# Optimization experiments

Hardware: AMD Instinct MI355X
Metric: run time of the kernel (lower is better)

## Reference

```python
import jax, jax.numpy as jnp
import numpy as np

TIME_NUM, WEEK_NUM = 288, 7
HID = 32          # hid_dim
T_OUT, IN_DIM = 12, 3
RF_DIM = 64       # random_feature_dim
TAU = 1.0
EPS_RF = 1e-6
EPS_LN = 1e-5


def _make_proj(m, d, seed=0):
    """Performer random matrix: stacked rows of QR-orthogonalized dxd blocks,
    scaled by chi-distributed row norms (create_random_matrix, scaling=0)."""
    rng = np.random.RandomState(seed)
    blocks = []
    for _ in range(m // d):
        q, _ = np.linalg.qr(rng.randn(d, d))
        blocks.append(q.T)
    rem = m - (m // d) * d
    if rem > 0:
        q, _ = np.linalg.qr(rng.randn(d, d))
        blocks.append(q.T[:rem])
    mat = np.vstack(blocks)
    mult = np.linalg.norm(rng.randn(m, d), axis=1)
    return jnp.asarray((mult[:, None] * mat).astype(np.float32))


def setup_inputs() -> dict:
    key = jax.random.key(0)
    B, N = 4, 50000
    ks = iter(jax.random.split(key, 40))
    rn = lambda *s: jax.random.normal(next(ks), s, jnp.float32) * 0.1
    inp = {
        "x": jax.random.uniform(next(ks), (B, N, T_OUT, IN_DIM), jnp.float32),
        "node_emb": rn(N, HID),
        "time_emb": rn(TIME_NUM, HID),
        "week_emb": rn(WEEK_NUM, HID),
        "W_in": rn(HID, T_OUT * IN_DIM), "b_in": rn(HID),
        "W1": rn(HID, 3 * HID), "b1": rn(HID),
        "W2": rn(HID, 3 * HID), "b2": rn(HID),
        "W_reg": rn(T_OUT, 8 * HID), "b_reg": rn(T_OUT),
        "proj": _make_proj(RF_DIM, HID, 0),
    }
    for i in range(2):
        inp[f"fc_in{i}_w"] = rn(4 * HID, 4 * HID)
        inp[f"fc_in{i}_b"] = rn(4 * HID)
        inp[f"fc_out{i}_w"] = rn(4 * HID, 4 * HID)
        inp[f"fc_out{i}_b"] = rn(4 * HID)
        inp[f"ln{i}_g"] = jnp.ones(4 * HID, jnp.float32)
        inp[f"ln{i}_b"] = jnp.zeros(4 * HID, jnp.float32)
    return inp


def _rf_map(data, proj, is_query):
    # data: [B,N,H,D], proj: [M,D] -> features [B,N,H,M]
    d = data.shape[-1]
    data = data * (float(d) ** -0.25)
    ratio = 1.0 / jnp.sqrt(jnp.asarray(proj.shape[0], data.dtype))
    dash = jnp.einsum('bnhd,md->bnhm', data, proj)
    diag = jnp.sum(data * data, -1, keepdims=True) * 0.5
    mx = jnp.max(dash, -1, keepdims=True)
    if not is_query:
        mx = jnp.max(mx, 1, keepdims=True)  # also max over nodes (dim -3)
    return ratio * (jnp.exp(dash - diag - mx) + EPS_RF)


def _linear_kernel(x, q, k):
    # x: [B,N,H,D], q/k: [B,N,H,M] -> O(N) kernelized attention
    v2x = jnp.einsum('bnhm,bnhd->bhmd', k, x)
    out1 = jnp.einsum('bnhm,bhmd->bnhd', q, v2x)
    ksum = jnp.sum(k, axis=1)                       # [B,H,M]
    out2 = jnp.einsum('bnhm,bhm->bnh', q, ksum)[..., None]
    return out1 / out2


def _layernorm(h, g, b):
    mu = jnp.mean(h, -1, keepdims=True)
    var = jnp.mean((h - mu) ** 2, -1, keepdims=True)
    return (h - mu) * jax.lax.rsqrt(var + EPS_LN) * g + b


def _forward(x, node_emb, time_emb, week_emb, W_in, b_in, W1, b1, W2, b2,
             W_reg, b_reg, proj,
             fc_in0_w, fc_in0_b, fc_out0_w, fc_out0_b, ln0_g, ln0_b,
             fc_in1_w, fc_in1_b, fc_out1_w, fc_out1_b, ln1_g, ln1_b):
    B, N, T, D = x.shape
    time_idx = jnp.clip((x[:, :, -1, 1] * TIME_NUM).astype(jnp.int32), 0, TIME_NUM - 1)
    week_idx = jnp.clip(x[:, :, -1, 2].astype(jnp.int32), 0, WEEK_NUM - 1)
    te = time_emb[time_idx]                                  # [B,N,H]
    we = week_emb[week_idx]                                  # [B,N,H]
    ne = jnp.broadcast_to(node_emb[None], (B, N, HID))       # [B,N,H]
    inp = x.reshape(B, N, T * D) @ W_in.T + b_in             # 1x1 conv == matmul
    xg = jnp.concatenate([ne, te, we], -1)                   # [B,N,3H]
    h = jnp.concatenate([inp, ne, te, we], -1)               # [B,N,4H]

    inv_sqrt_tau = 1.0 / float(np.sqrt(TAU))
    nv1 = ((xg @ W1.T + b1) * inv_sqrt_tau)[:, :, None, :]   # [B,N,1,H]
    nv2 = ((xg @ W2.T + b2) * inv_sqrt_tau)[:, :, None, :]
    q = _rf_map(nv1, proj, True)                             # [B,N,1,M]
    k = _rf_map(nv2, proj, False)

    layers = [(fc_in0_w, fc_in0_b, fc_out0_w, fc_out0_b, ln0_g, ln0_b),
              (fc_in1_w, fc_in1_b, fc_out1_w, fc_out1_b, ln1_g, ln1_b)]
    h0 = h
    for wi, bi, wo, bo, g, bt in layers:
        res = h
        v = jax.nn.sigmoid(h @ wi.T + bi) * (h @ wo.T + bo)  # GLU; dropout=eval
        v = _linear_kernel(v[:, :, None, :], q, k)[:, :, 0, :]
        h = _layernorm(v + res, g, bt)

    out = jax.nn.relu(jnp.concatenate([h0, h], -1))          # [B,N,8H]
    out = out @ W_reg.T + b_reg                              # [B,N,T_out]
    return jnp.swapaxes(out, 1, 2)                           # [B,T_out,N]


def reference(x, node_emb, time_emb, week_emb, W_in, b_in, W1, b1, W2, b2,
              W_reg, b_reg, proj,
              fc_in0_w, fc_in0_b, fc_out0_w, fc_out0_b, ln0_g, ln0_b,
              fc_in1_w, fc_in1_b, fc_out1_w, fc_out1_b, ln1_g, ln1_b):
    return _forward(x, node_emb, time_emb, week_emb, W_in, b_in, W1, b1, W2, b2,
                    W_reg, b_reg, proj,
                    fc_in0_w, fc_in0_b, fc_out0_w, fc_out0_b, ln0_g, ln0_b,
                    fc_in1_w, fc_in1_b, fc_out1_w, fc_out1_b, ln1_g, ln1_b)
```

## Files before the change

kernel.cpp:

```cpp
#include <hip/hip_runtime.h>

#define NB 4
#define NN 50000
#define NT 784

#define H0B    0L
#define H1B    51200000L
#define QB     102400000L
#define KKB    128000000L
#define RMB    153600000L
#define WBFB   154400000L
#define V2F0B  154531072L
#define V2F1B  154662144L
#define KSB    154793216L
#define GMB    154794240L
#define W12B   154795264L
#define V2TB   154819840L
#define NZERO  65796

typedef short short8_t __attribute__((ext_vector_type(8)));
typedef float f32x4 __attribute__((ext_vector_type(4)));

__device__ __forceinline__ unsigned short f2bf(float f){
  unsigned u = __float_as_uint(f);
  return (unsigned short)((u + 0x7FFFu + ((u>>16)&1u)) >> 16);
}
__device__ __forceinline__ float bf2f(unsigned short s){
  return __uint_as_float(((unsigned)s)<<16);
}
__device__ __forceinline__ unsigned pk2(float a, float b){
  return (unsigned)f2bf(a) | ((unsigned)f2bf(b)<<16);
}
__device__ __forceinline__ uint4 pk8(const float* f){
  uint4 o; o.x=pk2(f[0],f[1]); o.y=pk2(f[2],f[3]);
  o.z=pk2(f[4],f[5]); o.w=pk2(f[6],f[7]); return o;
}
__device__ __forceinline__ void up8(uint4 v, float* f){
  f[0]=bf2f((unsigned short)(v.x&0xFFFFu)); f[1]=bf2f((unsigned short)(v.x>>16));
  f[2]=bf2f((unsigned short)(v.y&0xFFFFu)); f[3]=bf2f((unsigned short)(v.y>>16));
  f[4]=bf2f((unsigned short)(v.z&0xFFFFu)); f[5]=bf2f((unsigned short)(v.z>>16));
  f[6]=bf2f((unsigned short)(v.w&0xFFFFu)); f[7]=bf2f((unsigned short)(v.w>>16));
}
__device__ __forceinline__ short8_t relu8(short8_t s){
  short8_t r;
  #pragma unroll
  for (int i=0;i<8;i++){ short v = s[i]; r[i] = (v & (short)0x8000) ? (short)0 : v; }
  return r;
}
__device__ __forceinline__ unsigned encOrd(float f){
  unsigned u = __float_as_uint(f);
  return (u & 0x80000000u) ? ~u : (u | 0x80000000u);
}
__device__ __forceinline__ float decOrd(unsigned u){
  return (u & 0x80000000u) ? __uint_as_float(u & 0x7fffffffu)
                           : __uint_as_float(~u);
}

__global__ void k_init(char* __restrict__ wsb){
  int i = blockIdx.x*256 + threadIdx.x;
  if (i < NZERO) ((unsigned*)(wsb + V2F0B))[i] = 0u;
}
__global__ void k_wcvt(const float* __restrict__ wi0, const float* __restrict__ wo0,
                       const float* __restrict__ wi1, const float* __restrict__ wo1,
                       char* __restrict__ wsb){
  int idx = blockIdx.x*256 + threadIdx.x;
  if (idx >= 65536) return;
  int l = idx >> 15, r = (idx >> 7) & 255, c = idx & 127;
  const float* src = (l==0) ? ((r<128)? wi0 : wo0) : ((r<128)? wi1 : wo1);
  float v = src[(r&127)*128 + c];
  ((unsigned short*)(wsb + WBFB))[l*32768 + r*128 + c] = f2bf(v);
}
__global__ void k_wcvt2(const float* __restrict__ W1, const float* __restrict__ W2,
                        const float* __restrict__ proj, const float* __restrict__ W_reg,
                        char* __restrict__ wsb){
  int i = blockIdx.x*256 + threadIdx.x;
  if (i >= 12288) return;
  unsigned short* dst = (unsigned short*)(wsb + W12B);
  float v;
  if (i < 3072) v = W1[i];
  else if (i < 6144) v = W2[i-3072];
  else if (i < 8192) v = proj[i-6144];
  else {
    int r = (i-8192) >> 8, c = (i-8192) & 255;
    v = (r < 12) ? W_reg[r*256 + c] : 0.f;
  }
  dst[i] = f2bf(v);
}

__global__ __launch_bounds__(256) void k_pass1a(
  const float* __restrict__ x, const float* __restrict__ node_emb,
  const float* __restrict__ time_emb, const float* __restrict__ week_emb,
  const float* __restrict__ W_in, const float* __restrict__ b_in,
  char* __restrict__ wsb)
{
  const int b = blockIdx.y;
  const int n = blockIdx.x*256 + threadIdx.x;
  if (n >= NN) return;
  const long row = (long)b*NN + n;
  float xr[36];
  {
    const float4* xp = (const float4*)(x + row*36);
    #pragma unroll
    for (int i=0;i<9;i++){ float4 t=xp[i]; xr[4*i]=t.x; xr[4*i+1]=t.y; xr[4*i+2]=t.z; xr[4*i+3]=t.w; }
  }
  int tidx = (int)(xr[34]*288.0f); tidx = tidx<0?0:(tidx>287?287:tidx);
  int widx = (int)(xr[35]);        widx = widx<0?0:(widx>6?6:widx);
  uint4* h0q = (uint4*)(wsb + H0B) + row*16;
  float hh[32];
  #pragma unroll 1
  for (int jj=0;jj<8;jj++){
    #pragma unroll
    for (int jl=0;jl<4;jl++){
      const int j = jj*4+jl;
      const float* w = W_in + j*36;
      float a0=0.f,a1=0.f,a2=0.f,a3=0.f;
      #pragma unroll
      for (int i=0;i<36;i+=4){ a0+=xr[i]*w[i]; a1+=xr[i+1]*w[i+1]; a2+=xr[i+2]*w[i+2]; a3+=xr[i+3]*w[i+3]; }
      hh[j] = b_in[j] + ((a0+a1)+(a2+a3));
    }
  }
  #pragma unroll
  for (int c=0;c<4;c++) h0q[c] = pk8(hh + 8*c);
  float xg[96];
  {
    const float4* p0 = (const float4*)(node_emb + (long)n*32);
    const float4* p1 = (const float4*)(time_emb + (long)tidx*32);
    const float4* p2 = (const float4*)(week_emb + (long)widx*32);
    #pragma unroll
    for (int i=0;i<8;i++){ float4 t=p0[i]; xg[4*i]=t.x; xg[4*i+1]=t.y; xg[4*i+2]=t.z; xg[4*i+3]=t.w; }
    #pragma unroll
    for (int i=0;i<8;i++){ float4 t=p1[i]; xg[32+4*i]=t.x; xg[32+4*i+1]=t.y; xg[32+4*i+2]=t.z; xg[32+4*i+3]=t.w; }
    #pragma unroll
    for (int i=0;i<8;i++){ float4 t=p2[i]; xg[64+4*i]=t.x; xg[64+4*i+1]=t.y; xg[64+4*i+2]=t.z; xg[64+4*i+3]=t.w; }
  }
  #pragma unroll
  for (int c=0;c<12;c++) h0q[4+c] = pk8(xg + 8*c);
}

__global__ __launch_bounds__(256) void k_pass1b(
  const float* __restrict__ b1, const float* __restrict__ b2,
  char* __restrict__ wsb)
{
  __shared__ unsigned short xgt[64][104];
  __shared__ unsigned short dt[2][64][40];
  __shared__ unsigned short ot[64][72];
  __shared__ unsigned short w1l[32][104];
  __shared__ unsigned short w2l[32][104];
  __shared__ unsigned short pjl[64][40];
  __shared__ float wred[4];
  const int b   = blockIdx.y;
  const int tid = threadIdx.x;
  const int lane= tid & 63;
  const int w   = tid >> 6;
  const int c   = lane & 15;
  const int kg  = lane >> 4;
  const int nblk = gridDim.x;
  const int srow = tid >> 2, sq3 = tid & 3;
  {
    const unsigned short* w1bf = (const unsigned short*)(wsb + W12B);
    const unsigned short* w2bf = w1bf + 3072;
    const unsigned short* pjbf = w1bf + 6144;
    for (int i = tid; i < 3072; i += 256){ w1l[i/96][i%96] = w1bf[i]; w2l[i/96][i%96] = w2bf[i]; }
    for (int i = tid; i < 2048; i += 256){ pjl[i/32][i%32] = pjbf[i]; }
  }
  uint4 xv0, xv1, xv2;
  {
    const long r0 = (long)blockIdx.x*64;
    long gr = r0 + srow;
    xv0=(uint4){0,0,0,0}; xv1=xv0; xv2=xv0;
    if (gr < NN){
      const uint4* src = (const uint4*)(wsb + H0B + ((long)b*NN + gr)*256 + 64 + sq3*48);
      xv0=src[0]; xv1=src[1]; xv2=src[2];
    }
  }
  #pragma unroll 1
  for (int tile = blockIdx.x; tile < NT; tile += nblk){
    const long r0blk = (long)tile*64;
    {
      uint4* d = (uint4*)&xgt[srow][sq3*24];
      d[0]=xv0; d[1]=xv1; d[2]=xv2;
    }
    if (tile + nblk < NT){
      const long r1 = (long)(tile + nblk)*64;
      long gr = r1 + srow;
      xv0=(uint4){0,0,0,0}; xv1=xv0; xv2=xv0;
      if (gr < NN){
        const uint4* src = (const uint4*)(wsb + H0B + ((long)b*NN + gr)*256 + 64 + sq3*48);
        xv0=src[0]; xv1=src[1]; xv2=src[2];
      }
    }
    __syncthreads();
    f32x4 accd[2][2];
    #pragma unroll
    for (int s=0;s<2;s++)
      #pragma unroll
      for (int f=0;f<2;f++) accd[s][f] = (f32x4){0.f,0.f,0.f,0.f};
    #pragma unroll
    for (int ks=0;ks<3;ks++){
      short8_t a = *(const short8_t*)&xgt[w*16 + c][ks*32 + kg*8];
      #pragma unroll
      for (int f=0;f<2;f++){
        short8_t bw1 = *(const short8_t*)&w1l[f*16+c][ks*32 + kg*8];
        accd[0][f] = __builtin_amdgcn_mfma_f32_16x16x32_bf16(a, bw1, accd[0][f], 0,0,0);
        short8_t bw2 = *(const short8_t*)&w2l[f*16+c][ks*32 + kg*8];
        accd[1][f] = __builtin_amdgcn_mfma_f32_16x16x32_bf16(a, bw2, accd[1][f], 0,0,0);
      }
    }
    const float DSC = 0.42044820762685725f;
    float dv[2][2][4];
    #pragma unroll
    for (int f=0;f<2;f++){
      float bb1 = b1[f*16+c], bb2 = b2[f*16+c];
      #pragma unroll
      for (int jj=0;jj<4;jj++){
        dv[0][f][jj] = (accd[0][f][jj] + bb1) * DSC;
        dv[1][f][jj] = (accd[1][f][jj] + bb2) * DSC;
      }
    }
    float dg[2][4];
    #pragma unroll
    for (int s=0;s<2;s++)
      #pragma unroll
      for (int jj=0;jj<4;jj++){
        float t = dv[s][0][jj]*dv[s][0][jj] + dv[s][1][jj]*dv[s][1][jj];
        #pragma unroll
        for (int off=1; off<16; off<<=1) t += __shfl_xor(t, off);
        dg[s][jj] = 0.5f * t;
      }
    #pragma unroll
    for (int s=0;s<2;s++)
      #pragma unroll
      for (int f=0;f<2;f++)
        #pragma unroll
        for (int jj=0;jj<4;jj++)
          dt[s][w*16 + kg*4 + jj][f*16 + c] = f2bf(dv[s][f][jj]);
    __syncthreads();
    f32x4 acc2[2][4];
    #pragma unroll
    for (int s=0;s<2;s++){
      short8_t ad = *(const short8_t*)&dt[s][w*16 + c][kg*8];
      #pragma unroll
      for (int f=0;f<4;f++){
        short8_t bp = *(const short8_t*)&pjl[f*16+c][kg*8];
        acc2[s][f] = __builtin_amdgcn_mfma_f32_16x16x32_bf16(ad, bp, (f32x4){0.f,0.f,0.f,0.f}, 0,0,0);
      }
    }
    float mx[2][4];
    #pragma unroll
    for (int s=0;s<2;s++)
      #pragma unroll
      for (int jj=0;jj<4;jj++){
        float t = fmaxf(fmaxf(acc2[s][0][jj],acc2[s][1][jj]),
                        fmaxf(acc2[s][2][jj],acc2[s][3][jj]));
        #pragma unroll
        for (int off=1; off<16; off<<=1) t = fmaxf(t, __shfl_xor(t, off));
        mx[s][jj] = t;
      }
    #pragma unroll
    for (int f=0;f<4;f++)
      #pragma unroll
      for (int jj=0;jj<4;jj++){
        float qv = 0.125f*(__expf(acc2[0][f][jj] - dg[0][jj] - mx[0][jj]) + 1e-6f);
        ot[w*16 + kg*4 + jj][f*16 + c] = f2bf(qv);
      }
    __syncthreads();
    {
      long gr = r0blk + srow;
      if (gr < NN){
        const uint4* s = (const uint4*)&ot[srow][sq3*16];
        uint4* dst = (uint4*)((unsigned short*)(wsb + QB) + ((long)b*NN + gr)*64 + sq3*16);
        dst[0] = s[0]; dst[1] = s[1];
      }
    }
    __syncthreads();
    float bmax = -3.0e38f;
    #pragma unroll
    for (int f=0;f<4;f++)
      #pragma unroll
      for (int jj=0;jj<4;jj++){
        float kv = __expf(acc2[1][f][jj] - mx[1][jj]);
        ot[w*16 + kg*4 + jj][f*16 + c] = f2bf(kv);
      }
    #pragma unroll
    for (int jj=0;jj<4;jj++){
      long gr = r0blk + w*16 + kg*4 + jj;
      bool val = (gr < NN);
      if (val && c==0)
        ((float*)(wsb + RMB))[(long)b*NN + gr] = mx[1][jj] - dg[1][jj];
      if (val) bmax = fmaxf(bmax, mx[1][jj]);
    }
    #pragma unroll
    for (int off=32; off>0; off>>=1) bmax = fmaxf(bmax, __shfl_xor(bmax, off));
    if (lane==0) wred[w] = bmax;
    __syncthreads();
    {
      long gr = r0blk + srow;
      if (gr < NN){
        const uint4* s = (const uint4*)&ot[srow][sq3*16];
        uint4* dst = (uint4*)((unsigned short*)(wsb + KKB) + ((long)b*NN + gr)*64 + sq3*16);
        dst[0] = s[0]; dst[1] = s[1];
      }
    }
    if (tid==0){
      float m2 = fmaxf(fmaxf(wred[0],wred[1]), fmaxf(wred[2],wred[3]));
      atomicMax((unsigned*)(wsb + GMB) + b, encOrd(m2));
    }
    __syncthreads();
  }
}

__global__ __launch_bounds__(256) void k_glured(
  char* __restrict__ wsb, const unsigned short* __restrict__ hsrc,
  const unsigned short* __restrict__ wbf,
  const float* __restrict__ bi, const float* __restrict__ bo,
  float* __restrict__ v2x_out, float* __restrict__ ksout)
{
  __shared__ unsigned short ht[64][132];
  __shared__ unsigned short htT[128][72];
  __shared__ unsigned short ktl[2][64][72];
  __shared__ float red[256];
  extern __shared__ unsigned short wl[];
  const int b = blockIdx.y;
  const int tid = threadIdx.x;
  const int lane = tid & 63;
  const int w = tid >> 6;
  const int c = lane & 15;
  const int kg = lane >> 4;
  const int nblk = gridDim.x;
  const float gm = decOrd(((const unsigned*)(wsb + GMB))[b]);
  const float* rm = (const float*)(wsb + RMB) + (long)b*NN;
  const uint4* kbase = (const uint4*)(wsb + KKB) + (long)b*NN*8;
  {
    uint4* wl4 = (uint4*)wl;
    const uint4* src = (const uint4*)wbf;
    #pragma unroll
    for (int e=0;e<16;e++){
      int i = tid + 256*e;
      int row = i >> 4, blk = i & 15;
      wl4[row*16 + (blk ^ (row & 7))] = src[i];
    }
  }
  f32x4 racc[8];
  #pragma unroll
  for (int f=0;f<8;f++) racc[f] = (f32x4){0.f,0.f,0.f,0.f};
  float ksacc = 0.f;
  float bi_l[8], bo_l[8];
  #pragma unroll
  for (int f=0;f<8;f++){ bi_l[f] = bi[f*16+c]; bo_l[f] = bo[f*16+c]; }
  const int krr = tid>>3, kcc = tid&7;
  const int srow = tid>>2, sq3 = tid&3;
  const int rswz = ((w*16 + c) >> 3) & 7;
  const int wswz = c & 7;
  uint4 hv0,hv1,hv2,hv3, krA,krB; float rmA,rmB;
  {
    const long r0 = (long)blockIdx.x*64;
    long gr = r0 + srow;
    hv0=(uint4){0,0,0,0}; hv1=hv0; hv2=hv0; hv3=hv0;
    if (gr < NN){
      const uint4* s = (const uint4*)(hsrc + ((long)b*NN + gr)*128 + sq3*32);
      hv0=s[0]; hv1=s[1]; hv2=s[2]; hv3=s[3];
    }
    krA=(uint4){0,0,0,0}; krB=krA; rmA=0.f; rmB=0.f;
    long gA = r0 + krr;      if (gA < NN){ krA = kbase[gA*8 + kcc]; rmA = rm[gA]; }
    long gB = r0 + krr + 32; if (gB < NN){ krB = kbase[gB*8 + kcc]; rmB = rm[gB]; }
  }
  int p = 0;
  #pragma unroll 1
  for (int tile = blockIdx.x; tile < NT; tile += nblk){
    const long r0 = (long)tile*64;
    {
      uint4* d = (uint4*)&ht[srow][sq3*32];
      d[0]=hv0; d[1]=hv1; d[2]=hv2; d[3]=hv3;
    }
    {
      bool vA = (r0 + krr) < NN;
      bool vB = (r0 + krr + 32) < NN;
      float sA = __expf(rmA - gm), sB = __expf(rmB - gm);
      float ta[8], tb[8];
      up8(krA, ta); up8(krB, tb);
      #pragma unroll
      for (int i=0;i<8;i++){
        ta[i] = vA ? 0.125f*(ta[i]*sA + 1e-6f) : 0.f;
        tb[i] = vB ? 0.125f*(tb[i]*sB + 1e-6f) : 0.f;
      }
      const int pA = (((krr>>3) ^ kcc) << 3) | (krr & 7);
      const int pB = ((((krr>>3)+4) ^ kcc) << 3) | (krr & 7);
      #pragma unroll
      for (int i=0;i<8;i++){
        ktl[p][kcc*8+i][pA] = f2bf(ta[i]);
        ktl[p][kcc*8+i][pB] = f2bf(tb[i]);
      }
    }
    if (tile + nblk < NT){
      const long r1 = (long)(tile + nblk)*64;
      long gr = r1 + srow;
      hv0=(uint4){0,0,0,0}; hv1=hv0; hv2=hv0; hv3=hv0;
      if (gr < NN){
        const uint4* s = (const uint4*)(hsrc + ((long)b*NN + gr)*128 + sq3*32);
        hv0=s[0]; hv1=s[1]; hv2=s[2]; hv3=s[3];
      }
      krA=(uint4){0,0,0,0}; krB=krA; rmA=0.f; rmB=0.f;
      long gA = r1 + krr;      if (gA < NN){ krA = kbase[gA*8 + kcc]; rmA = rm[gA]; }
      long gB = r1 + krr + 32; if (gB < NN){ krB = kbase[gB*8 + kcc]; rmB = rm[gB]; }
    }
    __syncthreads();
    f32x4 gacc[16];
    #pragma unroll
    for (int f=0;f<16;f++) gacc[f] = (f32x4){0.f,0.f,0.f,0.f};
    #pragma unroll
    for (int ks=0;ks<4;ks++){
      short8_t a = *(const short8_t*)&ht[w*16 + c][ks*32 + kg*8];
      #pragma unroll
      for (int f=0;f<16;f++){
        short8_t bb = *(const short8_t*)(wl + (((f*16 + c)*16 + ((ks*4 + kg) ^ wswz)) << 3));
        gacc[f] = __builtin_amdgcn_mfma_f32_16x16x32_bf16(a, bb, gacc[f], 0, 0, 0);
      }
    }
    #pragma unroll
    for (int f=0;f<8;f++)
      #pragma unroll
      for (int j=0;j<4;j++){
        float aa = gacc[f][j]   + bi_l[f];
        float cc2= gacc[f+8][j] + bo_l[f];
        float o  = cc2 / (1.0f + __expf(-aa));
        bool val = (r0 + w*16 + kg*4 + j) < NN;
        htT[f*16 + c][w*16 + kg*4 + j] = val ? f2bf(o) : (unsigned short)0;
      }
    if (ksout){
      int m = tid & 63, n0 = (tid>>6)*16;
      int sm = (m>>3)&7;
      #pragma unroll
      for (int n=0;n<16;n++){
        int nn = n0+n;
        ksacc += bf2f(ktl[p][m][(((nn>>3)^sm)<<3)|(nn&7)]);
      }
    }
    __syncthreads();
    #pragma unroll
    for (int ks=0;ks<2;ks++){
      short8_t a = *(const short8_t*)&ktl[p][w*16 + c][((ks*4 + kg) ^ rswz) << 3];
      #pragma unroll
      for (int f=0;f<8;f++){
        short8_t bb = *(const short8_t*)&htT[f*16 + c][ks*32 + kg*8];
        racc[f] = __builtin_amdgcn_mfma_f32_16x16x32_bf16(a, bb, racc[f], 0, 0, 0);
      }
    }
    p ^= 1;
  }
  float* v2x = v2x_out + (long)b*8192;
  #pragma unroll
  for (int f=0;f<8;f++)
    #pragma unroll
    for (int j=0;j<4;j++)
      atomicAdd(&v2x[(w*16 + kg*4 + j)*128 + f*16 + c], racc[f][j]);
  if (ksout){
    red[tid] = ksacc;
    __syncthreads();
    if (tid < 64)
      atomicAdd(ksout + b*64 + tid,
                red[tid]+red[64+tid]+red[128+tid]+red[192+tid]);
  }
}

__global__ void k_v2cvt(char* __restrict__ wsb, const float* __restrict__ v2f){
  int idx = blockIdx.x*256 + threadIdx.x;
  if (idx >= 36864) return;
  int b = idx / 9216, rem = idx % 9216;
  int n = rem / 64, m = rem % 64;
  const float* ks = (const float*)(wsb + KSB);
  float v = (n < 128) ? v2f[b*8192 + m*128 + n] : ((n==128) ? ks[b*64+m] : 0.f);
  ((unsigned short*)(wsb + V2TB))[b*9216 + n*64 + m] = f2bf(v);
}

__global__ __launch_bounds__(256) void k_attnln(
  char* __restrict__ wsb, const float* __restrict__ g0,
  const float* __restrict__ bt0)
{
  __shared__ unsigned short ht[64][132];
  __shared__ unsigned short v2s[144*72];
  const int b = blockIdx.y;
  const int tid = threadIdx.x;
  const int lane = tid & 63;
  const int w  = tid >> 6;
  const int c  = lane & 15;
  const int kg = lane >> 4;
  const int nblk = gridDim.x;
  const int rrow = tid>>2, rq3 = tid&3;
  const unsigned short* qb = (const unsigned short*)(wsb + QB) + (long)b*NN*64;
  const unsigned short* h0g = (const unsigned short*)(wsb + H0B) + (long)b*NN*128;
  unsigned short* h1g = (unsigned short*)(wsb + H1B) + (long)b*NN*128;
  {
    const uint4* v2g = (const uint4*)((const unsigned short*)(wsb + V2TB) + b*9216);
    #pragma unroll
    for (int e=0;e<5;e++){
      int j = tid + 256*e;
      if (j < 1152){
        int row = j >> 3, cc = j & 7;
        *(uint4*)&v2s[row*72 + cc*8] = v2g[j];
      }
    }
  }
  short8_t aq0, aq1;
  uint4 rh0, rh1, rh2, rh3;
  {
    const long r0 = (long)blockIdx.x*64;
    if (r0 + w*16 + c < NN){
      const unsigned short* qrow = qb + (r0 + w*16 + c)*64 + kg*8;
      aq0 = *(const short8_t*)qrow; aq1 = *(const short8_t*)(qrow + 32);
    } else { aq0 = (short8_t){0,0,0,0,0,0,0,0}; aq1 = aq0; }
    rh0=(uint4){0,0,0,0}; rh1=rh0; rh2=rh0; rh3=rh0;
    if (r0 + rrow < NN){
      const uint4* hs = (const uint4*)(h0g + (r0 + rrow)*128 + rq3*32);
      rh0=hs[0]; rh1=hs[1]; rh2=hs[2]; rh3=hs[3];
    }
  }
  __syncthreads();
  #pragma unroll 1
  for (int tile = blockIdx.x; tile < NT; tile += nblk){
    const long r0blk = (long)tile*64;
    const long rgr = r0blk + rrow;
    f32x4 acc[9];
    #pragma unroll
    for (int f=0;f<9;f++) acc[f] = (f32x4){0.f,0.f,0.f,0.f};
    #pragma unroll
    for (int f=0;f<9;f++){
      short8_t b0 = *(const short8_t*)&v2s[(f*16 + c)*72 + kg*8];
      acc[f] = __builtin_amdgcn_mfma_f32_16x16x32_bf16(aq0, b0, acc[f], 0, 0, 0);
      short8_t b1v = *(const short8_t*)&v2s[(f*16 + c)*72 + 32 + kg*8];
      acc[f] = __builtin_amdgcn_mfma_f32_16x16x32_bf16(aq1, b1v, acc[f], 0, 0, 0);
    }
    float inv[4];
    #pragma unroll
    for (int j=0;j<4;j++) inv[j] = 1.0f / __shfl(acc[8][j], (lane & 48));
    #pragma unroll
    for (int f=0;f<8;f++)
      #pragma unroll
      for (int j=0;j<4;j++)
        ht[w*16 + kg*4 + j][f*16 + c] = f2bf(acc[f][j]*inv[j]);
    __syncthreads();
    short8_t aq0n, aq1n;
    uint4 nh0, nh1, nh2, nh3;
    {
      aq0n = (short8_t){0,0,0,0,0,0,0,0}; aq1n = aq0n;
      nh0=(uint4){0,0,0,0}; nh1=nh0; nh2=nh0; nh3=nh0;
      if (tile + nblk < NT){
        const long r1 = (long)(tile + nblk)*64;
        if (r1 + w*16 + c < NN){
          const unsigned short* qrow = qb + (r1 + w*16 + c)*64 + kg*8;
          aq0n = *(const short8_t*)qrow; aq1n = *(const short8_t*)(qrow + 32);
        }
        if (r1 + rrow < NN){
          const uint4* hs = (const uint4*)(h0g + (r1 + rrow)*128 + rq3*32);
          nh0=hs[0]; nh1=hs[1]; nh2=hs[2]; nh3=hs[3];
        }
      }
    }
    {
      float tv[32];
      {
        const uint4* os = (const uint4*)&ht[rrow][rq3*32];
        uint4 o0=os[0],o1=os[1],o2=os[2],o3=os[3];
        up8(o0,tv); up8(o1,tv+8); up8(o2,tv+16); up8(o3,tv+24);
      }
      {
        float hv[32];
        up8(rh0,hv); up8(rh1,hv+8); up8(rh2,hv+16); up8(rh3,hv+24);
        #pragma unroll
        for (int i=0;i<32;i++) tv[i] += hv[i];
      }
      float s = 0.f;
      #pragma unroll
      for (int i=0;i<32;i++) s += tv[i];
      s += __shfl_xor(s, 1); s += __shfl_xor(s, 2);
      float mu = s * (1.0f/128.0f);
      float vv = 0.f;
      #pragma unroll
      for (int i=0;i<32;i++){ float e = tv[i]-mu; vv += e*e; }
      vv += __shfl_xor(vv, 1); vv += __shfl_xor(vv, 2);
      float rs = rsqrtf(vv * (1.0f/128.0f) + 1e-5f);
      const float4* gp = (const float4*)(g0 + rq3*32);
      const float4* bp = (const float4*)(bt0 + rq3*32);
      float h1v[32];
      #pragma unroll
      for (int i8=0;i8<8;i8++){
        float4 g4 = gp[i8], b4 = bp[i8];
        h1v[i8*4  ] = (tv[i8*4  ]-mu)*rs*g4.x + b4.x;
        h1v[i8*4+1] = (tv[i8*4+1]-mu)*rs*g4.y + b4.y;
        h1v[i8*4+2] = (tv[i8*4+2]-mu)*rs*g4.z + b4.z;
        h1v[i8*4+3] = (tv[i8*4+3]-mu)*rs*g4.w + b4.w;
      }
      if (rgr < NN){
        uint4 p0=pk8(h1v), p1=pk8(h1v+8), p2=pk8(h1v+16), p3=pk8(h1v+24);
        uint4* dst = (uint4*)(h1g + rgr*128 + rq3*32);
        dst[0]=p0; dst[1]=p1; dst[2]=p2; dst[3]=p3;
      }
    }
    __syncthreads();
    aq0=aq0n; aq1=aq1n; rh0=nh0; rh1=nh1; rh2=nh2; rh3=nh3;
  }
}

__global__ __launch_bounds__(256) void k_attnhead(
  char* __restrict__ wsb, const float* __restrict__ g1,
  const float* __restrict__ bt1, const float* __restrict__ b_reg,
  float* __restrict__ out)
{
  __shared__ unsigned short ht[64][132];
  __shared__ unsigned short v2s[144*72];
  __shared__ unsigned short h0t[64][136];
  __shared__ unsigned short wrl[16][264];
  const int b = blockIdx.y;
  const int tid = threadIdx.x;
  const int lane = tid & 63;
  const int w  = tid >> 6;
  const int c  = lane & 15;
  const int kg = lane >> 4;
  const int nblk = gridDim.x;
  const int rrow = tid>>2, rq3 = tid&3;
  const unsigned short* qb  = (const unsigned short*)(wsb + QB) + (long)b*NN*64;
  const unsigned short* h0g = (const unsigned short*)(wsb + H0B) + (long)b*NN*128;
  const unsigned short* h1g = (const unsigned short*)(wsb + H1B) + (long)b*NN*128;
  {
    const uint4* v2g = (const uint4*)((const unsigned short*)(wsb + V2TB) + b*9216);
    #pragma unroll
    for (int e=0;e<5;e++){
      int j = tid + 256*e;
      if (j < 1152){
        int row = j >> 3, cc = j & 7;
        *(uint4*)&v2s[row*72 + cc*8] = v2g[j];
      }
    }
    const unsigned short* wregT = (const unsigned short*)(wsb + W12B) + 8192;
    for (int i = tid; i < 4096; i += 256)
      wrl[i>>8][i&255] = wregT[i];
  }
  short8_t aq0, aq1;
  uint4 rh0, rh1, rh2, rh3, ah0, ah1, ah2, ah3;
  {
    const long r0 = (long)blockIdx.x*64;
    if (r0 + w*16 + c < NN){
      const unsigned short* qrow = qb + (r0 + w*16 + c)*64 + kg*8;
      aq0 = *(const short8_t*)qrow; aq1 = *(const short8_t*)(qrow + 32);
    } else { aq0 = (short8_t){0,0,0,0,0,0,0,0}; aq1 = aq0; }
    rh0=(uint4){0,0,0,0}; rh1=rh0; rh2=rh0; rh3=rh0;
    ah0=rh0; ah1=rh0; ah2=rh0; ah3=rh0;
    if (r0 + rrow < NN){
      const uint4* hs = (const uint4*)(h1g + (r0 + rrow)*128 + rq3*32);
      rh0=hs[0]; rh1=hs[1]; rh2=hs[2]; rh3=hs[3];
      const uint4* h0s = (const uint4*)(h0g + (r0 + rrow)*128 + rq3*32);
      ah0=h0s[0]; ah1=h0s[1]; ah2=h0s[2]; ah3=h0s[3];
    }
  }
  __syncthreads();
  #pragma unroll 1
  for (int tile = blockIdx.x; tile < NT; tile += nblk){
    const long r0blk = (long)tile*64;
    const long r0w = r0blk + w*16;
    const long rgr = r0blk + rrow;
    f32x4 acc[9];
    #pragma unroll
    for (int f=0;f<9;f++) acc[f] = (f32x4){0.f,0.f,0.f,0.f};
    #pragma unroll
    for (int f=0;f<9;f++){
      short8_t b0 = *(const short8_t*)&v2s[(f*16 + c)*72 + kg*8];
      acc[f] = __builtin_amdgcn_mfma_f32_16x16x32_bf16(aq0, b0, acc[f], 0, 0, 0);
      short8_t b1v = *(const short8_t*)&v2s[(f*16 + c)*72 + 32 + kg*8];
      acc[f] = __builtin_amdgcn_mfma_f32_16x16x32_bf16(aq1, b1v, acc[f], 0, 0, 0);
    }
    float inv[4];
    #pragma unroll
    for (int j=0;j<4;j++) inv[j] = 1.0f / __shfl(acc[8][j], (lane & 48));
    #pragma unroll
    for (int f=0;f<8;f++)
      #pragma unroll
      for (int j=0;j<4;j++)
        ht[w*16 + kg*4 + j][f*16 + c] = f2bf(acc[f][j]*inv[j]);
    __syncthreads();
    short8_t aq0n, aq1n;
    uint4 nh0, nh1, nh2, nh3, na0, na1, na2, na3;
    {
      aq0n = (short8_t){0,0,0,0,0,0,0,0}; aq1n = aq0n;
      nh0=(uint4){0,0,0,0}; nh1=nh0; nh2=nh0; nh3=nh0;
      na0=nh0; na1=nh0; na2=nh0; na3=nh0;
      if (tile + nblk < NT){
        const long r1 = (long)(tile + nblk)*64;
        if (r1 + w*16 + c < NN){
          const unsigned short* qrow = qb + (r1 + w*16 + c)*64 + kg*8;
          aq0n = *(const short8_t*)qrow; aq1n = *(const short8_t*)(qrow + 32);
        }
        if (r1 + rrow < NN){
          const uint4* hs = (const uint4*)(h1g + (r1 + rrow)*128 + rq3*32);
          nh0=hs[0]; nh1=hs[1]; nh2=hs[2]; nh3=hs[3];
          const uint4* h0s = (const uint4*)(h0g + (r1 + rrow)*128 + rq3*32);
          na0=h0s[0]; na1=h0s[1]; na2=h0s[2]; na3=h0s[3];
        }
      }
    }
    {
      uint4* hd = (uint4*)&h0t[rrow][rq3*32];
      hd[0]=ah0; hd[1]=ah1; hd[2]=ah2; hd[3]=ah3;
      float tv[32];
      {
        const uint4* os = (const uint4*)&ht[rrow][rq3*32];
        uint4 o0=os[0],o1=os[1],o2=os[2],o3=os[3];
        up8(o0,tv); up8(o1,tv+8); up8(o2,tv+16); up8(o3,tv+24);
      }
      {
        float hv[32];
        up8(rh0,hv); up8(rh1,hv+8); up8(rh2,hv+16); up8(rh3,hv+24);
        #pragma unroll
        for (int i=0;i<32;i++) tv[i] += hv[i];
      }
      float s = 0.f;
      #pragma unroll
      for (int i=0;i<32;i++) s += tv[i];
      s += __shfl_xor(s, 1); s += __shfl_xor(s, 2);
      float mu = s * (1.0f/128.0f);
      float vv = 0.f;
      #pragma unroll
      for (int i=0;i<32;i++){ float e = tv[i]-mu; vv += e*e; }
      vv += __shfl_xor(vv, 1); vv += __shfl_xor(vv, 2);
      float rs = rsqrtf(vv * (1.0f/128.0f) + 1e-5f);
      const float4* gp = (const float4*)(g1 + rq3*32);
      const float4* bp = (const float4*)(bt1 + rq3*32);
      float h2v[32];
      #pragma unroll
      for (int i8=0;i8<8;i8++){
        float4 g4 = gp[i8], b4 = bp[i8];
        h2v[i8*4  ] = fmaxf((tv[i8*4  ]-mu)*rs*g4.x + b4.x, 0.f);
        h2v[i8*4+1] = fmaxf((tv[i8*4+1]-mu)*rs*g4.y + b4.y, 0.f);
        h2v[i8*4+2] = fmaxf((tv[i8*4+2]-mu)*rs*g4.z + b4.z, 0.f);
        h2v[i8*4+3] = fmaxf((tv[i8*4+3]-mu)*rs*g4.w + b4.w, 0.f);
      }
      uint4 p0=pk8(h2v), p1=pk8(h2v+8), p2=pk8(h2v+16), p3=pk8(h2v+24);
      uint4* d = (uint4*)&ht[rrow][rq3*32];
      d[0]=p0; d[1]=p1; d[2]=p2; d[3]=p3;
    }
    __syncthreads();
    f32x4 hacc = (f32x4){0.f,0.f,0.f,0.f};
    #pragma unroll
    for (int ks=0;ks<8;ks++){
      short8_t a;
      if (ks < 4)
        a = relu8(*(const short8_t*)&h0t[w*16 + c][ks*32 + kg*8]);
      else
        a = *(const short8_t*)&ht[w*16 + c][(ks-4)*32 + kg*8];
      short8_t bb = *(const short8_t*)&wrl[c][ks*32 + kg*8];
      hacc = __builtin_amdgcn_mfma_f32_16x16x32_bf16(a, bb, hacc, 0, 0, 0);
    }
    if (c < 12){
      float br = b_reg[c];
      #pragma unroll
      for (int j=0;j<4;j++){
        long gr = r0w + kg*4 + j;
        if (gr < NN)
          out[((long)b*12 + c)*NN + gr] = hacc[j] + br;
      }
    }
    __syncthreads();
    aq0=aq0n; aq1=aq1n;
    rh0=nh0; rh1=nh1; rh2=nh2; rh3=nh3;
    ah0=na0; ah1=na1; ah2=na2; ah3=na3;
  }
}

extern "C" void kernel_launch(void* const* d_in, const int* in_sizes, int n_in,
                              void* d_out, int out_size, void* d_ws, size_t ws_size,
                              hipStream_t stream)
{
  const float* x        = (const float*)d_in[0];
  const float* node_emb = (const float*)d_in[1];
  const float* time_emb = (const float*)d_in[2];
  const float* week_emb = (const float*)d_in[3];
  const float* W_in     = (const float*)d_in[4];
  const float* b_in     = (const float*)d_in[5];
  const float* W1       = (const float*)d_in[6];
  const float* b1       = (const float*)d_in[7];
  const float* W2       = (const float*)d_in[8];
  const float* b2       = (const float*)d_in[9];
  const float* W_reg    = (const float*)d_in[10];
  const float* b_reg    = (const float*)d_in[11];
  const float* proj     = (const float*)d_in[12];
  const float* fc_in0_w = (const float*)d_in[13];
  const float* fc_in0_b = (const float*)d_in[14];
  const float* fc_out0_w= (const float*)d_in[15];
  const float* fc_out0_b= (const float*)d_in[16];
  const float* ln0_g    = (const float*)d_in[17];
  const float* ln0_b    = (const float*)d_in[18];
  const float* fc_in1_w = (const float*)d_in[19];
  const float* fc_in1_b = (const float*)d_in[20];
  const float* fc_out1_w= (const float*)d_in[21];
  const float* fc_out1_b= (const float*)d_in[22];
  const float* ln1_g    = (const float*)d_in[23];
  const float* ln1_b    = (const float*)d_in[24];
  char* wsb  = (char*)d_ws;
  float* out = (float*)d_out;

  dim3 rowgrid((NN+255)/256, NB);
  dim3 pgrid(128, NB);
  dim3 cvtgrid(144);

  hipFuncSetAttribute((const void*)k_glured,
                      hipFuncAttributeMaxDynamicSharedMemorySize, 65536);

  k_init  <<<258, 256, 0, stream>>>(wsb);
  k_wcvt  <<<256, 256, 0, stream>>>(fc_in0_w, fc_out0_w, fc_in1_w, fc_out1_w, wsb);
  k_wcvt2 <<<48, 256, 0, stream>>>(W1, W2, proj, W_reg, wsb);
  k_pass1a<<<rowgrid, 256, 0, stream>>>(x, node_emb, time_emb, week_emb,
                                        W_in, b_in, wsb);
  k_pass1b<<<pgrid, 256, 0, stream>>>(b1, b2, wsb);
  k_glured<<<pgrid, 256, 65536, stream>>>(wsb, (const unsigned short*)(wsb + H0B),
                                          (const unsigned short*)(wsb + WBFB),
                                          fc_in0_b, fc_out0_b,
                                          (float*)(wsb + V2F0B), (float*)(wsb + KSB));
  k_v2cvt <<<cvtgrid, 256, 0, stream>>>(wsb, (const float*)(wsb + V2F0B));
  k_attnln<<<pgrid, 256, 0, stream>>>(wsb, ln0_g, ln0_b);
  k_glured<<<pgrid, 256, 65536, stream>>>(wsb, (const unsigned short*)(wsb + H1B),
                                          (const unsigned short*)(wsb + WBFB) + 32768,
                                          fc_in1_b, fc_out1_b,
                                          (float*)(wsb + V2F1B), (float*)nullptr);
  k_v2cvt <<<cvtgrid, 256, 0, stream>>>(wsb, (const float*)(wsb + V2F1B));
  k_attnhead<<<pgrid, 256, 0, stream>>>(wsb, ln1_g, ln1_b, b_reg, out);
}
```

Baseline: 363.6 us.

## Split k_glured across 512 threads with waves partitioning output feature columns

Doubles the k_glured block to 512 threads (8 waves). Each wave now covers a 16-row slice and half of the GLU output features, so per-thread accumulators drop from 16+8 to 8+4 MFMA tiles. The grid is halved to 64 blocks per batch, so each block walks twice as many tiles. The aim is to cut register pressure and spread the per-tile MFMA and global-load work over more waves per CU. The cost is fewer blocks overall, a shared weight copy per larger block, and more threads contending at each barrier.

```diff
diff --git a/kernel.cpp b/kernel.cpp
--- a/kernel.cpp
+++ b/kernel.cpp
@@ -309,7 +309,7 @@
   }
 }
 
-__global__ __launch_bounds__(256) void k_glured(
+__global__ __launch_bounds__(512) void k_glured(
   char* __restrict__ wsb, const unsigned short* __restrict__ hsrc,
   const unsigned short* __restrict__ wbf,
   const float* __restrict__ bi, const float* __restrict__ bo,
@@ -318,13 +318,15 @@
   __shared__ unsigned short ht[64][132];
   __shared__ unsigned short htT[128][72];
   __shared__ unsigned short ktl[2][64][72];
-  __shared__ float red[256];
+  __shared__ float red[512];
   extern __shared__ unsigned short wl[];
   const int b = blockIdx.y;
   const int tid = threadIdx.x;
   const int lane = tid & 63;
-  const int w = tid >> 6;
-  const int c = lane & 15;
+  const int w  = tid >> 6;
+  const int wr = w & 3;
+  const int wh = w >> 2;
+  const int c  = lane & 15;
   const int kg = lane >> 4;
   const int nblk = gridDim.x;
   const float gm = decOrd(((const unsigned*)(wsb + GMB))[b]);
@@ -334,103 +336,108 @@
     uint4* wl4 = (uint4*)wl;
     const uint4* src = (const uint4*)wbf;
     #pragma unroll
-    for (int e=0;e<16;e++){
-      int i = tid + 256*e;
+    for (int e=0;e<8;e++){
+      int i = tid + 512*e;
       int row = i >> 4, blk = i & 15;
       wl4[row*16 + (blk ^ (row & 7))] = src[i];
     }
   }
-  f32x4 racc[8];
+  f32x4 racc[4];
   #pragma unroll
-  for (int f=0;f<8;f++) racc[f] = (f32x4){0.f,0.f,0.f,0.f};
+  for (int f=0;f<4;f++) racc[f] = (f32x4){0.f,0.f,0.f,0.f};
   float ksacc = 0.f;
-  float bi_l[8], bo_l[8];
+  float bi_l[4], bo_l[4];
   #pragma unroll
-  for (int f=0;f<8;f++){ bi_l[f] = bi[f*16+c]; bo_l[f] = bo[f*16+c]; }
+  for (int ff=0;ff<4;ff++){
+    bi_l[ff] = bi[(wh*4+ff)*16 + c];
+    bo_l[ff] = bo[(wh*4+ff)*16 + c];
+  }
   const int krr = tid>>3, kcc = tid&7;
-  const int srow = tid>>2, sq3 = tid&3;
-  const int rswz = ((w*16 + c) >> 3) & 7;
+  const int srow = tid>>3, sq = tid&7;
+  const int rswz = ((wr*16 + c) >> 3) & 7;
   const int wswz = c & 7;
-  uint4 hv0,hv1,hv2,hv3, krA,krB; float rmA,rmB;
+  uint4 hv0,hv1, krA; float rmA;
   {
     const long r0 = (long)blockIdx.x*64;
     long gr = r0 + srow;
-    hv0=(uint4){0,0,0,0}; hv1=hv0; hv2=hv0; hv3=hv0;
+    hv0=(uint4){0,0,0,0}; hv1=hv0;
     if (gr < NN){
-      const uint4* s = (const uint4*)(hsrc + ((long)b*NN + gr)*128 + sq3*32);
-      hv0=s[0]; hv1=s[1]; hv2=s[2]; hv3=s[3];
-    }
-    krA=(uint4){0,0,0,0}; krB=krA; rmA=0.f; rmB=0.f;
-    long gA = r0 + krr;      if (gA < NN){ krA = kbase[gA*8 + kcc]; rmA = rm[gA]; }
-    long gB = r0 + krr + 32; if (gB < NN){ krB = kbase[gB*8 + kcc]; rmB = rm[gB]; }
+      const uint4* s = (const uint4*)(hsrc + ((long)b*NN + gr)*128 + sq*16);
+      hv0=s[0]; hv1=s[1];
+    }
+    krA=(uint4){0,0,0,0}; rmA=0.f;
+    long gA = r0 + krr;
+    if (gA < NN){ krA = kbase[gA*8 + kcc]; rmA = rm[gA]; }
   }
   int p = 0;
   #pragma unroll 1
   for (int tile = blockIdx.x; tile < NT; tile += nblk){
     const long r0 = (long)tile*64;
     {
-      uint4* d = (uint4*)&ht[srow][sq3*32];
-      d[0]=hv0; d[1]=hv1; d[2]=hv2; d[3]=hv3;
+      uint4* d = (uint4*)&ht[srow][sq*16];
+      d[0]=hv0; d[1]=hv1;
     }
     {
       bool vA = (r0 + krr) < NN;
-      bool vB = (r0 + krr + 32) < NN;
-      float sA = __expf(rmA - gm), sB = __expf(rmB - gm);
-      float ta[8], tb[8];
-      up8(krA, ta); up8(krB, tb);
-      #pragma unroll
-      for (int i=0;i<8;i++){
+      float sA = __expf(rmA - gm);
+      float ta[8];
+      up8(krA, ta);
+      #pragma unroll
+      for (int i=0;i<8;i++)
         ta[i] = vA ? 0.125f*(ta[i]*sA + 1e-6f) : 0.f;
-        tb[i] = vB ? 0.125f*(tb[i]*sB + 1e-6f) : 0.f;
-      }
       const int pA = (((krr>>3) ^ kcc) << 3) | (krr & 7);
-      const int pB = ((((krr>>3)+4) ^ kcc) << 3) | (krr & 7);
-      #pragma unroll
-      for (int i=0;i<8;i++){
+      #pragma unroll
+      for (int i=0;i<8;i++)
         ktl[p][kcc*8+i][pA] = f2bf(ta[i]);
-        ktl[p][kcc*8+i][pB] = f2bf(tb[i]);
-      }
     }
     if (tile + nblk < NT){
       const long r1 = (long)(tile + nblk)*64;
       long gr = r1 + srow;
-      hv0=(uint4){0,0,0,0}; hv1=hv0; hv2=hv0; hv3=hv0;
+      hv0=(uint4){0,0,0,0}; hv1=hv0;
       if (gr < NN){
-        const uint4* s = (const uint4*)(hsrc + ((long)b*NN + gr)*128 + sq3*32);
-        hv0=s[0]; hv1=s[1]; hv2=s[2]; hv3=s[3];
-      }
-      krA=(uint4){0,0,0,0}; krB=krA; rmA=0.f; rmB=0.f;
-      long gA = r1 + krr;      if (gA < NN){ krA = kbase[gA*8 + kcc]; rmA = rm[gA]; }
-      long gB = r1 + krr + 32; if (gB < NN){ krB = kbase[gB*8 + kcc]; rmB = rm[gB]; }
-    }
-    __syncthreads();
-    f32x4 gacc[16];
-    #pragma unroll
-    for (int f=0;f<16;f++) gacc[f] = (f32x4){0.f,0.f,0.f,0.f};
-    #pragma unroll
-    for (int ks=0;ks<4;ks++){
-      short8_t a = *(const short8_t*)&ht[w*16 + c][ks*32 + kg*8];
-      #pragma unroll
-      for (int f=0;f<16;f++){
-        short8_t bb = *(const short8_t*)(wl + (((f*16 + c)*16 + ((ks*4 + kg) ^ wswz)) << 3));
-        gacc[f] = __builtin_amdgcn_mfma_f32_16x16x32_bf16(a, bb, gacc[f], 0, 0, 0);
-      }
-    }
-    #pragma unroll
-    for (int f=0;f<8;f++)
-      #pragma unroll
-      for (int j=0;j<4;j++){
-        float aa = gacc[f][j]   + bi_l[f];
-        float cc2= gacc[f+8][j] + bo_l[f];
-        float o  = cc2 / (1.0f + __expf(-aa));
-        bool val = (r0 + w*16 + kg*4 + j) < NN;
-        htT[f*16 + c][w*16 + kg*4 + j] = val ? f2bf(o) : (unsigned short)0;
-      }
+        const uint4* s = (const uint4*)(hsrc + ((long)b*NN + gr)*128 + sq*16);
+        hv0=s[0]; hv1=s[1];
+      }
+      krA=(uint4){0,0,0,0}; rmA=0.f;
+      long gA = r1 + krr;
+      if (gA < NN){ krA = kbase[gA*8 + kcc]; rmA = rm[gA]; }
+    }
+    __syncthreads();
+    {
+      const f32x4 z4 = (f32x4){0.f,0.f,0.f,0.f};
+      f32x4 gi[4], go[4];
+      #pragma unroll
+      for (int ff=0;ff<4;ff++){ gi[ff]=z4; go[ff]=z4; }
+      #pragma unroll
+      for (int ks=0;ks<4;ks++){
+        short8_t a = *(const short8_t*)&ht[wr*16 + c][ks*32 + kg*8];
+        #pragma unroll
+        for (int ff=0;ff<4;ff++){
+          const int fi = wh*4 + ff;
+          short8_t bwi = *(const short8_t*)(wl + (((fi*16 + c)*16 + ((ks*4 + kg) ^ wswz)) << 3));
+          gi[ff] = __builtin_amdgcn_mfma_f32_16x16x32_bf16(a, bwi, gi[ff], 0, 0, 0);
+          short8_t bwo = *(const short8_t*)(wl + ((((fi+8)*16 + c)*16 + ((ks*4 + kg) ^ wswz)) << 3));
+          go[ff] = __builtin_amdgcn_mfma_f32_16x16x32_bf16(a, bwo, go[ff], 0, 0, 0);
+        }
+      }
+      #pragma unroll
+      for (int ff=0;ff<4;ff++){
+        const int fi = wh*4 + ff;
+        #pragma unroll
+        for (int j=0;j<4;j++){
+          float aa = gi[ff][j] + bi_l[ff];
+          float cc2= go[ff][j] + bo_l[ff];
+          float o  = cc2 / (1.0f + __expf(-aa));
+          bool val = (r0 + wr*16 + kg*4 + j) < NN;
+          htT[fi*16 + c][wr*16 + kg*4 + j] = val ? f2bf(o) : (unsigned short)0;
+        }
+      }
+    }
     if (ksout){
-      int m = tid & 63, n0 = (tid>>6)*16;
+      int m = tid & 63, n0 = (tid>>6)*8;
       int sm = (m>>3)&7;
       #pragma unroll
-      for (int n=0;n<16;n++){
+      for (int n=0;n<8;n++){
         int nn = n0+n;
         ksacc += bf2f(ktl[p][m][(((nn>>3)^sm)<<3)|(nn&7)]);
       }
@@ -438,27 +445,31 @@
     __syncthreads();
     #pragma unroll
     for (int ks=0;ks<2;ks++){
-      short8_t a = *(const short8_t*)&ktl[p][w*16 + c][((ks*4 + kg) ^ rswz) << 3];
-      #pragma unroll
-      for (int f=0;f<8;f++){
-        short8_t bb = *(const short8_t*)&htT[f*16 + c][ks*32 + kg*8];
-        racc[f] = __builtin_amdgcn_mfma_f32_16x16x32_bf16(a, bb, racc[f], 0, 0, 0);
+      short8_t a = *(const short8_t*)&ktl[p][wr*16 + c][((ks*4 + kg) ^ rswz) << 3];
+      #pragma unroll
+      for (int ff=0;ff<4;ff++){
+        const int fi = wh*4 + ff;
+        short8_t bb = *(const short8_t*)&htT[fi*16 + c][ks*32 + kg*8];
+        racc[ff] = __builtin_amdgcn_mfma_f32_16x16x32_bf16(a, bb, racc[ff], 0, 0, 0);
       }
     }
     p ^= 1;
   }
   float* v2x = v2x_out + (long)b*8192;
   #pragma unroll
-  for (int f=0;f<8;f++)
+  for (int ff=0;ff<4;ff++)
     #pragma unroll
     for (int j=0;j<4;j++)
-      atomicAdd(&v2x[(w*16 + kg*4 + j)*128 + f*16 + c], racc[f][j]);
+      atomicAdd(&v2x[(wr*16 + kg*4 + j)*128 + (wh*4+ff)*16 + c], racc[ff][j]);
   if (ksout){
     red[tid] = ksacc;
     __syncthreads();
-    if (tid < 64)
-      atomicAdd(ksout + b*64 + tid,
-                red[tid]+red[64+tid]+red[128+tid]+red[192+tid]);
+    if (tid < 64){
+      float s = 0.f;
+      #pragma unroll
+      for (int q=0;q<8;q++) s += red[q*64 + tid];
+      atomicAdd(ksout + b*64 + tid, s);
+    }
   }
 }
 
@@ -798,6 +809,7 @@
 
   dim3 rowgrid((NN+255)/256, NB);
   dim3 pgrid(128, NB);
+  dim3 ggrid(64, NB);
   dim3 cvtgrid(144);
 
   hipFuncSetAttribute((const void*)k_glured,
@@ -809,13 +821,13 @@
   k_pass1a<<<rowgrid, 256, 0, stream>>>(x, node_emb, time_emb, week_emb,
                                         W_in, b_in, wsb);
   k_pass1b<<<pgrid, 256, 0, stream>>>(b1, b2, wsb);
-  k_glured<<<pgrid, 256, 65536, stream>>>(wsb, (const unsigned short*)(wsb + H0B),
+  k_glured<<<ggrid, 512, 65536, stream>>>(wsb, (const unsigned short*)(wsb + H0B),
                                           (const unsigned short*)(wsb + WBFB),
                                           fc_in0_b, fc_out0_b,
                                           (float*)(wsb + V2F0B), (float*)(wsb + KSB));
   k_v2cvt <<<cvtgrid, 256, 0, stream>>>(wsb, (const float*)(wsb + V2F0B));
   k_attnln<<<pgrid, 256, 0, stream>>>(wsb, ln0_g, ln0_b);
-  k_glured<<<pgrid, 256, 65536, stream>>>(wsb, (const unsigned short*)(wsb + H1B),
+  k_glured<<<ggrid, 512, 65536, stream>>>(wsb, (const unsigned short*)(wsb + H1B),
                                           (const unsigned short*)(wsb + WBFB) + 32768,
                                           fc_in1_b, fc_out1_b,
                                           (float*)(wsb + V2F1B), (float*)nullptr);
```

Result: faster. 320.5 us (-11.9%).
